# Performance work log

Hardware: AMD Instinct MI355X
Metric: run time of the kernel (lower is better)

Reference implementation:

```python
import jax, jax.numpy as jnp
import numpy as np

DT = 1.0
EPS = 1e-6


def setup_inputs() -> dict:
    key = jax.random.key(0)
    k1, k2, k3, k4 = jax.random.split(key, 4)
    batch, in_ch, out_ch, state_dim, T = 16, 256, 256, 256, 8192
    u = jax.random.normal(k1, (batch, in_ch, T), dtype=jnp.float32)
    raw_lambda = jax.random.normal(k2, (state_dim,), dtype=jnp.float32)
    B_c = jax.random.normal(k3, (in_ch, state_dim), dtype=jnp.float32) * (1.0 / in_ch ** 0.5)
    C = jax.random.normal(k4, (state_dim, out_ch), dtype=jnp.float32) * (1.0 / state_dim ** 0.5)
    return {"u": u, "raw_lambda": raw_lambda, "B_c": B_c, "C": C}


def reference(u, raw_lambda, B_c, C):
    # ZOH discretization of diagonal SSM (all-real here since raw_lambda is real)
    lam = -jax.nn.softplus(raw_lambda)                 # (N,)
    A_d = jnp.exp(lam * DT)                            # (N,)
    factor = jnp.where(jnp.abs(lam) > EPS, (A_d - 1.0) / lam, jnp.full_like(lam, DT))
    B_d = B_c * factor[None, :]                        # (in_ch, N)

    # Precompute driving inputs for every step in one big GEMM: (T, B, N)
    x = jnp.einsum('bct,cn->tbn', u, B_d)

    batch, state_dim = u.shape[0], raw_lambda.shape[0]

    def step(s, x_t):
        s = s * A_d[None, :] + x_t                     # diagonal recurrence
        return s, s

    s0 = jnp.zeros((batch, state_dim), dtype=u.dtype)
    _, states = jax.lax.scan(step, s0, x)              # states: (T, B, N)

    # Project all states at once: y (B, out_ch, T)
    y = jnp.einsum('tbn,no->bot', states, C)
    return y
```

## Files before the change

kernel.cpp:

```cpp
#include <hip/hip_runtime.h>
#include <math.h>

typedef __attribute__((ext_vector_type(4)))  float f32x4;
typedef __attribute__((ext_vector_type(8)))  short short8;
typedef __attribute__((ext_vector_type(16))) float f32x16;

#define B_  16
#define C_  256
#define N_  256
#define O_  256
#define T_  8192
#define L_  64
#define NC_ 128

#define GLL16(gptr, lptr) \
  __builtin_amdgcn_global_load_lds((const __attribute__((address_space(1))) void*)(gptr), \
                                   (__attribute__((address_space(3))) void*)(lptr), 16, 0, 0)

__device__ inline unsigned short f2bf(float x) {
    unsigned u = __float_as_uint(x);
    u += 0x7fff + ((u >> 16) & 1);
    return (unsigned short)(u >> 16);
}
__device__ inline float bf2f(unsigned short h) {
    return __uint_as_float(((unsigned)h) << 16);
}
__device__ inline unsigned cvtpk(float a, float b) {
    unsigned r;
    asm("v_cvt_pk_bf16_f32 %0, %1, %2" : "=v"(r) : "v"(a), "v"(b));
    return r;
}
__device__ inline f32x16 zero16() {
    f32x16 z;
    #pragma unroll
    for (int i = 0; i < 16; ++i) z[i] = 0.f;
    return z;
}

__global__ __launch_bounds__(256) void k_prep(
    const float* __restrict__ raw_lambda, const float* __restrict__ B_c,
    const float* __restrict__ Cmat,
    float* __restrict__ Ad, float* __restrict__ AL,
    unsigned short* __restrict__ BdKf, unsigned short* __restrict__ CKf)
{
    const int r = blockIdx.x;
    const int t = threadIdx.x;
    const int kk = r >> 5, ri = r & 31;
    const int s = ri >> 4, hi = (ri >> 3) & 1, j = ri & 7;
    const int nt = t >> 5, l = (hi << 5) | (t & 31);
    const int idx = (((kk * 8 + nt) * 2 + s) * 64 + l) * 8 + j;

    if (blockIdx.y == 0) {
        const float x  = raw_lambda[t];
        const float sp = (x > 20.f) ? x : log1pf(expf(x));
        const float lam = -sp;
        const float ad  = expf(lam);
        const float factor = (fabsf(lam) > 1e-6f) ? (ad - 1.f) / lam : 1.f;
        if (r == 0) {
            Ad[t] = ad;
            float al = ad;
            #pragma unroll
            for (int i = 0; i < 6; ++i) al *= al;
            AL[t] = al;
        }
        BdKf[idx] = f2bf(B_c[r * N_ + t] * factor);
    } else {
        CKf[idx] = f2bf(Cmat[r * O_ + t]);
    }
}

#define LDFRAG(MAT, kk, buf) { \
    _Pragma("unroll") \
    for (int q_ = 0; q_ < 2; ++q_) \
        _Pragma("unroll") \
        for (int s_ = 0; s_ < 2; ++s_) \
            fb[buf][q_ * 2 + s_] = *(const short8*)( \
                (MAT) + ((((kk) * 8 + 2 * w + q_) * 2 + s_) * 64 + l) * 8); }

__global__ __launch_bounds__(256, 3) void k_phaseA(
    const float* __restrict__ u, const unsigned short* __restrict__ BdKf,
    const float* __restrict__ Ad, float* __restrict__ p_last,
    unsigned short* __restrict__ X, int doX)
{
    __shared__ __align__(16) unsigned short ut[16896];

    const int k = blockIdx.x, b = blockIdx.y;
    const int tid = threadIdx.x;
    const int w = tid >> 6, l = tid & 63, lo = l & 31, hi = l >> 5;
    const float* ub = u + (size_t)b * C_ * T_ + k * L_;

    const float adq0 = Ad[(2 * w + 0) * 32 + lo];
    const float adq1 = Ad[(2 * w + 1) * 32 + lo];

    {
        f32x4 va[8], vb[8];
        #pragma unroll
        for (int q = 0; q < 8; ++q) {
            const int idx = q * 256 + tid;
            const int p = idx >> 4, t4 = idx & 15;
            const float* base = ub + (size_t)(2 * p) * T_ + t4 * 4;
            va[q] = __builtin_nontemporal_load((const f32x4*)(base));
            vb[q] = __builtin_nontemporal_load((const f32x4*)(base + T_));
        }
        unsigned* ud = (unsigned*)ut;
        #pragma unroll
        for (int q = 0; q < 8; ++q) {
            const int idx = q * 256 + tid;
            const int p = idx >> 4, t4 = idx & 15;
            const int nb = p >> 2, jd = p & 3;
            #pragma unroll
            for (int r = 0; r < 4; ++r) {
                const int tA = 4 * t4 + r;
                const int xsw = (tA >> 3) & 3;
                ud[tA * 132 + (((nb ^ xsw) << 2) | jd)] = cvtpk(va[q][r], vb[q][r]);
            }
        }
    }
    __syncthreads();

    f32x16 a00 = zero16(), a01 = zero16(), a10 = zero16(), a11 = zero16();
    {
        short8 fb[3][4];
        LDFRAG(BdKf, 0, 0)
        LDFRAG(BdKf, 1, 1)
        #pragma unroll
        for (int kk = 0; kk < 8; ++kk) {
            if (kk < 6) LDFRAG(BdKf, kk + 2, (kk + 2) % 3)
            #pragma unroll
            for (int s = 0; s < 2; ++s) {
                const int blk8 = kk * 4 + s * 2 + hi;
                const int tA2 = lo, tB2 = 32 + lo;
                const short8 fa0 = *(const short8*)(ut + tA2 * 264 + ((blk8 ^ ((tA2 >> 3) & 3)) << 3));
                const short8 fa1 = *(const short8*)(ut + tB2 * 264 + ((blk8 ^ ((tB2 >> 3) & 3)) << 3));
                const short8 fb0 = fb[kk % 3][0 * 2 + s];
                const short8 fb1 = fb[kk % 3][1 * 2 + s];
                a00 = __builtin_amdgcn_mfma_f32_32x32x16_bf16(fa0, fb0, a00, 0, 0, 0);
                a01 = __builtin_amdgcn_mfma_f32_32x32x16_bf16(fa0, fb1, a01, 0, 0, 0);
                a10 = __builtin_amdgcn_mfma_f32_32x32x16_bf16(fa1, fb0, a10, 0, 0, 0);
                a11 = __builtin_amdgcn_mfma_f32_32x32x16_bf16(fa1, fb1, a11, 0, 0, 0);
            }
        }
    }

    if (doX) {
        unsigned* Xd = (unsigned*)X + (size_t)(k * B_ + b) * 8192;
        #pragma unroll
        for (int f = 0; f < 4; ++f) {
            const f32x16 a = (f == 0) ? a00 : (f == 1) ? a01 : (f == 2) ? a10 : a11;
            unsigned dw[8];
            #pragma unroll
            for (int d = 0; d < 8; ++d)
                dw[d] = cvtpk(a[2 * d], a[2 * d + 1]);
            unsigned* base = Xd + w * 2048 + f * 512 + l * 4;
            *(int4*)(base)       = *(const int4*)&dw[0];
            *(int4*)(base + 256) = *(const int4*)&dw[4];
        }
    }

    {
        float p[2];
        #pragma unroll
        for (int q = 0; q < 2; ++q) {
            const float ad = q ? adq1 : adq0;
            const float ad2 = ad * ad, ad4 = ad2 * ad2, ad8 = ad4 * ad4;
            const float ad16 = ad8 * ad8, ad32 = ad16 * ad16;
            float full[2];
            #pragma unroll
            for (int tt = 0; tt < 2; ++tt) {
                const f32x16 a = (tt == 0) ? (q == 0 ? a00 : a01)
                                           : (q == 0 ? a10 : a11);
                float v2[4];
                #pragma unroll
                for (int g = 0; g < 4; ++g)
                    v2[g] = fmaf(fmaf(fmaf(a[4*g], ad, a[4*g+1]), ad, a[4*g+2]), ad, a[4*g+3]);
                const float H = fmaf(fmaf(fmaf(v2[0], ad8, v2[1]), ad8, v2[2]), ad8, v2[3]);
                float P = hi ? H : H * ad4;
                P += __shfl_xor(P, 32);
                full[tt] = P;
            }
            p[q] = fmaf(full[0], ad32, full[1]);
        }
        if (hi == 0) {
            float* dst = p_last + (size_t)(k * B_ + b) * N_;
            dst[(2 * w + 0) * 32 + lo] = p[0];
            dst[(2 * w + 1) * 32 + lo] = p[1];
        }
    }
}

__global__ __launch_bounds__(256) void k_phaseB(
    const float* __restrict__ p_last, const float* __restrict__ AL,
    float* __restrict__ carry)
{
    __shared__ float buf[32 * 256];
    const int b = blockIdx.x, n = threadIdx.x;
    const float al = AL[n];
    float cur = 0.f;
    for (int kc = 0; kc < 4; ++kc) {
        __syncthreads();
        #pragma unroll
        for (int q = 0; q < 32; ++q)
            buf[q * 256 + n] = p_last[((size_t)(kc * 32 + q) * B_ + b) * N_ + n];
        __syncthreads();
        #pragma unroll
        for (int q = 0; q < 32; ++q) {
            carry[((size_t)(kc * 32 + q) * B_ + b) * N_ + n] = cur;
            cur = fmaf(cur, al, buf[q * 256 + n]);
        }
    }
}

__global__ __launch_bounds__(256, 3) void k_phaseC(
    const unsigned short* __restrict__ X, const unsigned short* __restrict__ CKf,
    const float* __restrict__ Ad, const float* __restrict__ carry,
    float* __restrict__ y)
{
    __shared__ __align__(16) unsigned short xs[16896];

    const int k = blockIdx.x, b = blockIdx.y;
    const int tid = threadIdx.x;
    const int w = tid >> 6, l = tid & 63, lo = l & 31, hi = l >> 5;
    const int t0 = k * L_;

    {
        const char* src = (const char*)X + (size_t)(k * B_ + b) * 32768;
        #pragma unroll
        for (int q = 0; q < 8; ++q)
            GLL16(src + q * 4096 + w * 1024 + (l << 4),
                  (char*)xs + q * 4096 + w * 1024);
    }
    const float cv = carry[(size_t)(k * B_ + b) * N_ + tid];
    const float ad = Ad[tid];
    __syncthreads();

    unsigned arr[2][2][8];
    {
        const unsigned* xd = (const unsigned*)xs;
        const int w2 = tid >> 6, q2 = (tid >> 5) & 1, lo2 = tid & 31;
        #pragma unroll
        for (int tt = 0; tt < 2; ++tt)
            #pragma unroll
            for (int h2 = 0; h2 < 2; ++h2) {
                const unsigned* p = xd + w2 * 2048 + (tt * 2 + q2) * 512
                                       + (h2 * 32 + lo2) * 4;
                *(int4*)&arr[tt][h2][0] = *(const int4*)(p);
                *(int4*)&arr[tt][h2][4] = *(const int4*)(p + 256);
            }
    }
    __syncthreads();

    {
        const int nb = tid >> 3, nl = tid & 7;
        float s = cv;
        #pragma unroll
        for (int tt = 0; tt < 2; ++tt)
            #pragma unroll
            for (int g = 0; g < 4; ++g)
                #pragma unroll
                for (int h2 = 0; h2 < 2; ++h2) {
                    const unsigned d0 = arr[tt][h2][2 * g];
                    const unsigned d1 = arr[tt][h2][2 * g + 1];
                    const int tb = tt * 32 + 8 * g + 4 * h2;
                    const int swz = (((nb ^ ((tb >> 3) & 3)) << 3) | nl);
                    s = fmaf(s, ad, bf2f((unsigned short)(d0 & 0xffff)));
                    xs[(tb + 0) * 264 + swz] = f2bf(s);
                    s = fmaf(s, ad, bf2f((unsigned short)(d0 >> 16)));
                    xs[(tb + 1) * 264 + swz] = f2bf(s);
                    s = fmaf(s, ad, bf2f((unsigned short)(d1 & 0xffff)));
                    xs[(tb + 2) * 264 + swz] = f2bf(s);
                    s = fmaf(s, ad, bf2f((unsigned short)(d1 >> 16)));
                    xs[(tb + 3) * 264 + swz] = f2bf(s);
                }
    }
    __syncthreads();

    f32x16 c00 = zero16(), c01 = zero16(), c10 = zero16(), c11 = zero16();
    {
        short8 fb[3][4];
        LDFRAG(CKf, 0, 0)
        LDFRAG(CKf, 1, 1)
        #pragma unroll
        for (int kk = 0; kk < 8; ++kk) {
            if (kk < 6) LDFRAG(CKf, kk + 2, (kk + 2) % 3)
            #pragma unroll
            for (int s = 0; s < 2; ++s) {
                short8 fa[2];
                #pragma unroll
                for (int tt = 0; tt < 2; ++tt) {
                    const int t = tt * 32 + lo;
                    const int blk = (kk * 4 + s * 2 + hi) ^ ((t >> 3) & 3);
                    fa[tt] = *(const short8*)(xs + t * 264 + blk * 8);
                }
                const short8 fb0 = fb[kk % 3][0 * 2 + s];
                const short8 fb1 = fb[kk % 3][1 * 2 + s];
                c00 = __builtin_amdgcn_mfma_f32_32x32x16_bf16(fa[0], fb0, c00, 0, 0, 0);
                c01 = __builtin_amdgcn_mfma_f32_32x32x16_bf16(fa[0], fb1, c01, 0, 0, 0);
                c10 = __builtin_amdgcn_mfma_f32_32x32x16_bf16(fa[1], fb0, c10, 0, 0, 0);
                c11 = __builtin_amdgcn_mfma_f32_32x32x16_bf16(fa[1], fb1, c11, 0, 0, 0);
            }
        }
    }

    #pragma unroll
    for (int tt = 0; tt < 2; ++tt)
        #pragma unroll
        for (int q = 0; q < 2; ++q) {
            const f32x16 a = (tt == 0) ? (q == 0 ? c00 : c01) : (q == 0 ? c10 : c11);
            const int o = (2 * w + q) * 32 + lo;
            float* yo = y + ((size_t)b * O_ + o) * T_ + t0 + tt * 32 + hi * 4;
            #pragma unroll
            for (int g = 0; g < 4; ++g) {
                float4 vv;
                vv.x = a[g * 4 + 0]; vv.y = a[g * 4 + 1];
                vv.z = a[g * 4 + 2]; vv.w = a[g * 4 + 3];
                *(float4*)(yo + g * 8) = vv;
            }
        }
}

__device__ __forceinline__ void gemm1_rc(
    const float* __restrict__ u, const unsigned short* __restrict__ BdKf,
    int b, int k, unsigned short* xs, unsigned short* ut, unsigned short* bb)
{
    const int tid = threadIdx.x;
    const int w = tid >> 6, l = tid & 63, lo = l & 31, hi = l >> 5;
    const int t0 = k * L_;
    f32x16 a00 = zero16(), a01 = zero16(), a10 = zero16(), a11 = zero16();
    for (int kk = 0; kk < 8; ++kk) {
        #pragma unroll
        for (int q = 0; q < 2; ++q) {
            const int i = q * 256 + tid, cl = i >> 4, t4 = i & 15;
            const float4 v = *(const float4*)(
                u + ((size_t)b * C_ + kk * 32 + cl) * T_ + t0 + t4 * 4);
            ut[(t4 * 4 + 0) * 40 + cl] = f2bf(v.x);
            ut[(t4 * 4 + 1) * 40 + cl] = f2bf(v.y);
            ut[(t4 * 4 + 2) * 40 + cl] = f2bf(v.z);
            ut[(t4 * 4 + 3) * 40 + cl] = f2bf(v.w);
        }
        {
            const unsigned short* src = BdKf + kk * 8192;
            #pragma unroll
            for (int q = 0; q < 4; ++q) {
                const int i16 = q * 256 + tid;
                *(int4*)(bb + i16 * 8) = *(const int4*)(src + i16 * 8);
            }
        }
        __syncthreads();
        #pragma unroll
        for (int s = 0; s < 2; ++s) {
            const short8 fa0 = *(const short8*)(ut + (0 * 32 + lo) * 40 + s * 16 + hi * 8);
            const short8 fa1 = *(const short8*)(ut + (1 * 32 + lo) * 40 + s * 16 + hi * 8);
            const short8 fb0 = *(const short8*)(bb + (((2 * w + 0) * 2 + s) * 64 + l) * 8);
            const short8 fb1 = *(const short8*)(bb + (((2 * w + 1) * 2 + s) * 64 + l) * 8);
            a00 = __builtin_amdgcn_mfma_f32_32x32x16_bf16(fa0, fb0, a00, 0, 0, 0);
            a01 = __builtin_amdgcn_mfma_f32_32x32x16_bf16(fa0, fb1, a01, 0, 0, 0);
            a10 = __builtin_amdgcn_mfma_f32_32x32x16_bf16(fa1, fb0, a10, 0, 0, 0);
            a11 = __builtin_amdgcn_mfma_f32_32x32x16_bf16(fa1, fb1, a11, 0, 0, 0);
        }
        __syncthreads();
    }
    #pragma unroll
    for (int tt = 0; tt < 2; ++tt)
        #pragma unroll
        for (int q = 0; q < 2; ++q) {
            const f32x16 a = (tt == 0) ? (q == 0 ? a00 : a01) : (q == 0 ? a10 : a11);
            const int n = (2 * w + q) * 32 + lo;
            #pragma unroll
            for (int g = 0; g < 4; ++g)
                #pragma unroll
                for (int p = 0; p < 2; ++p)
                    *(unsigned*)(xs + n * 66 + tt * 32 + hi * 4 + g * 8 + p * 2)
                        = f2bf(a[g * 4 + 2 * p]) | ((unsigned)f2bf(a[g * 4 + 2 * p + 1]) << 16);
        }
    __syncthreads();
}

__global__ __launch_bounds__(256) void k_phaseC_rc(
    const float* __restrict__ u, const unsigned short* __restrict__ BdKf,
    const unsigned short* __restrict__ CKf, const float* __restrict__ Ad,
    const float* __restrict__ carry, float* __restrict__ y)
{
    __shared__ __align__(16) unsigned short xs[16896];
    __shared__ __align__(16) unsigned short ut[2560];
    __shared__ __align__(16) unsigned short bb[8192];

    const int k = blockIdx.x, b = blockIdx.y;
    const int tid = threadIdx.x;
    const int w = tid >> 6, l = tid & 63, lo = l & 31, hi = l >> 5;
    const int t0 = k * L_;

    gemm1_rc(u, BdKf, b, k, xs, ut, bb);

    {
        const float a = Ad[tid];
        float s = carry[((size_t)k * B_ + b) * N_ + tid];
        float st[64];
        #pragma unroll
        for (int m = 0; m < 32; ++m) {
            const unsigned dw = *(const unsigned*)(xs + tid * 66 + 2 * m);
            s = fmaf(s, a, bf2f((unsigned short)(dw & 0xffff)));  st[2 * m] = s;
            s = fmaf(s, a, bf2f((unsigned short)(dw >> 16)));     st[2 * m + 1] = s;
        }
        __syncthreads();
        #pragma unroll
        for (int t = 0; t < 64; ++t) xs[t * 264 + tid] = f2bf(st[t]);
    }
    __syncthreads();

    f32x16 c00 = zero16(), c01 = zero16(), c10 = zero16(), c11 = zero16();
    for (int kk = 0; kk < 8; ++kk) {
        __syncthreads();
        {
            const unsigned short* src = CKf + kk * 8192;
            #pragma unroll
            for (int q = 0; q < 4; ++q) {
                const int i16 = q * 256 + tid;
                *(int4*)(bb + i16 * 8) = *(const int4*)(src + i16 * 8);
            }
        }
        __syncthreads();
        #pragma unroll
        for (int s = 0; s < 2; ++s) {
            const short8 fa0 = *(const short8*)(xs + (0 * 32 + lo) * 264 + kk * 32 + s * 16 + hi * 8);
            const short8 fa1 = *(const short8*)(xs + (1 * 32 + lo) * 264 + kk * 32 + s * 16 + hi * 8);
            const short8 fb0 = *(const short8*)(bb + (((2 * w + 0) * 2 + s) * 64 + l) * 8);
            const short8 fb1 = *(const short8*)(bb + (((2 * w + 1) * 2 + s) * 64 + l) * 8);
            c00 = __builtin_amdgcn_mfma_f32_32x32x16_bf16(fa0, fb0, c00, 0, 0, 0);
            c01 = __builtin_amdgcn_mfma_f32_32x32x16_bf16(fa0, fb1, c01, 0, 0, 0);
            c10 = __builtin_amdgcn_mfma_f32_32x32x16_bf16(fa1, fb0, c10, 0, 0, 0);
            c11 = __builtin_amdgcn_mfma_f32_32x32x16_bf16(fa1, fb1, c11, 0, 0, 0);
        }
    }

    #pragma unroll
    for (int tt = 0; tt < 2; ++tt)
        #pragma unroll
        for (int q = 0; q < 2; ++q) {
            const f32x16 a = (tt == 0) ? (q == 0 ? c00 : c01) : (q == 0 ? c10 : c11);
            const int o = (2 * w + q) * 32 + lo;
            float* yo = y + ((size_t)b * O_ + o) * T_ + t0 + tt * 32 + hi * 4;
            #pragma unroll
            for (int g = 0; g < 4; ++g) {
                float4 vv;
                vv.x = a[g * 4 + 0]; vv.y = a[g * 4 + 1];
                vv.z = a[g * 4 + 2]; vv.w = a[g * 4 + 3];
                *(float4*)(yo + g * 8) = vv;
            }
        }
}

extern "C" void kernel_launch(void* const* d_in, const int* in_sizes, int n_in,
                              void* d_out, int out_size, void* d_ws, size_t ws_size,
                              hipStream_t stream)
{
    const float* u  = (const float*)d_in[0];
    const float* rl = (const float*)d_in[1];
    const float* Bc = (const float*)d_in[2];
    const float* Cm = (const float*)d_in[3];
    float* y  = (float*)d_out;
    char*  ws = (char*)d_ws;

    float* Ad     = (float*)(ws + 0);
    float* AL     = (float*)(ws + 1024);
    float* p_last = (float*)(ws + 2048);
    float* carry  = (float*)(ws + 2048 + 2097152);
    unsigned short* BdKf = (unsigned short*)(ws + 2048 + 2 * 2097152);
    unsigned short* CKf  = (unsigned short*)(ws + 2048 + 2 * 2097152 + 131072);
    unsigned short* X    = (unsigned short*)(ws + 2048 + 2 * 2097152 + 2 * 131072);
    const size_t need = 2048 + 2ull * 2097152 + 2ull * 131072
                      + (size_t)NC_ * B_ * 32768;
    const int doX = (ws_size >= need) ? 1 : 0;

    k_prep  <<<dim3(256, 2),  dim3(256), 0, stream>>>(rl, Bc, Cm, Ad, AL, BdKf, CKf);
    k_phaseA<<<dim3(NC_, B_), dim3(256), 0, stream>>>(u, BdKf, Ad, p_last, X, doX);
    k_phaseB<<<dim3(B_),      dim3(256), 0, stream>>>(p_last, AL, carry);
    if (doX)
        k_phaseC<<<dim3(NC_, B_), dim3(256), 0, stream>>>(X, CKf, Ad, carry, y);
    else
        k_phaseC_rc<<<dim3(NC_, B_), dim3(256), 0, stream>>>(u, BdKf, CKf, Ad, carry, y);
}
```

Baseline: 102.6 us.

## Warp-specialize phase A with double-buffered LDS over four chunks per block

Phase A now uses 512-thread blocks, where half the waves load and pack u into LDS while the other half run the MFMA GEMM and the X and p_last epilogues. Each block processes four consecutive chunks with a double-buffered LDS tile. The aim is to overlap the global loads of u with tensor-core compute and epilogue stores. The trade-offs are a grid four times smaller, more LDS per block, and a sync per chunk, which may reduce overall memory parallelism.

```diff
diff --git a/kernel.cpp b/kernel.cpp
--- a/kernel.cpp
+++ b/kernel.cpp
@@ -12,6 +12,7 @@
 #define T_  8192
 #define L_  64
 #define NC_ 128
+#define CH_ 4
 
 #define GLL16(gptr, lptr) \
   __builtin_amdgcn_global_load_lds((const __attribute__((address_space(1))) void*)(gptr), \
@@ -77,35 +78,33 @@
             fb[buf][q_ * 2 + s_] = *(const short8*)( \
                 (MAT) + ((((kk) * 8 + 2 * w + q_) * 2 + s_) * 64 + l) * 8); }
 
-__global__ __launch_bounds__(256, 3) void k_phaseA(
+__global__ __launch_bounds__(512) void k_phaseA(
     const float* __restrict__ u, const unsigned short* __restrict__ BdKf,
     const float* __restrict__ Ad, float* __restrict__ p_last,
     unsigned short* __restrict__ X, int doX)
 {
-    __shared__ __align__(16) unsigned short ut[16896];
-
-    const int k = blockIdx.x, b = blockIdx.y;
+    __shared__ __align__(16) unsigned short ut[2][16896];
+
+    const int k0 = blockIdx.x * CH_, b = blockIdx.y;
     const int tid = threadIdx.x;
-    const int w = tid >> 6, l = tid & 63, lo = l & 31, hi = l >> 5;
-    const float* ub = u + (size_t)b * C_ * T_ + k * L_;
-
-    const float adq0 = Ad[(2 * w + 0) * 32 + lo];
-    const float adq1 = Ad[(2 * w + 1) * 32 + lo];
-
-    {
+    const bool loader = tid < 256;
+    const float* ub = u + (size_t)b * C_ * T_ + k0 * L_;
+
+    const int lt = tid;
+    auto load_pack = [&](int chunk, unsigned short* dst) {
         f32x4 va[8], vb[8];
         #pragma unroll
         for (int q = 0; q < 8; ++q) {
-            const int idx = q * 256 + tid;
+            const int idx = q * 256 + lt;
             const int p = idx >> 4, t4 = idx & 15;
-            const float* base = ub + (size_t)(2 * p) * T_ + t4 * 4;
+            const float* base = ub + (size_t)(2 * p) * T_ + chunk * L_ + t4 * 4;
             va[q] = __builtin_nontemporal_load((const f32x4*)(base));
             vb[q] = __builtin_nontemporal_load((const f32x4*)(base + T_));
         }
-        unsigned* ud = (unsigned*)ut;
+        unsigned* ud = (unsigned*)dst;
         #pragma unroll
         for (int q = 0; q < 8; ++q) {
-            const int idx = q * 256 + tid;
+            const int idx = q * 256 + lt;
             const int p = idx >> 4, t4 = idx & 15;
             const int nb = p >> 2, jd = p & 3;
             #pragma unroll
@@ -115,11 +114,18 @@
                 ud[tA * 132 + (((nb ^ xsw) << 2) | jd)] = cvtpk(va[q][r], vb[q][r]);
             }
         }
-    }
-    __syncthreads();
-
-    f32x16 a00 = zero16(), a01 = zero16(), a10 = zero16(), a11 = zero16();
-    {
+    };
+
+    const int ct = tid - 256;
+    const int w = (ct >> 6) & 3, l = ct & 63, lo = l & 31, hi = l >> 5;
+    float adq0 = 0.f, adq1 = 0.f;
+    if (!loader) {
+        adq0 = Ad[(2 * w + 0) * 32 + lo];
+        adq1 = Ad[(2 * w + 1) * 32 + lo];
+    }
+
+    auto gemm = [&](const unsigned short* src,
+                    f32x16& a00, f32x16& a01, f32x16& a10, f32x16& a11) {
         short8 fb[3][4];
         LDFRAG(BdKf, 0, 0)
         LDFRAG(BdKf, 1, 1)
@@ -130,8 +136,8 @@
             for (int s = 0; s < 2; ++s) {
                 const int blk8 = kk * 4 + s * 2 + hi;
                 const int tA2 = lo, tB2 = 32 + lo;
-                const short8 fa0 = *(const short8*)(ut + tA2 * 264 + ((blk8 ^ ((tA2 >> 3) & 3)) << 3));
-                const short8 fa1 = *(const short8*)(ut + tB2 * 264 + ((blk8 ^ ((tB2 >> 3) & 3)) << 3));
+                const short8 fa0 = *(const short8*)(src + tA2 * 264 + ((blk8 ^ ((tA2 >> 3) & 3)) << 3));
+                const short8 fa1 = *(const short8*)(src + tB2 * 264 + ((blk8 ^ ((tB2 >> 3) & 3)) << 3));
                 const short8 fb0 = fb[kk % 3][0 * 2 + s];
                 const short8 fb1 = fb[kk % 3][1 * 2 + s];
                 a00 = __builtin_amdgcn_mfma_f32_32x32x16_bf16(fa0, fb0, a00, 0, 0, 0);
@@ -140,13 +146,14 @@
                 a11 = __builtin_amdgcn_mfma_f32_32x32x16_bf16(fa1, fb1, a11, 0, 0, 0);
             }
         }
-    }
-
-    if (doX) {
+    };
+
+    auto xstore = [&](const f32x16& a00, const f32x16& a01,
+                      const f32x16& a10, const f32x16& a11, int k) {
         unsigned* Xd = (unsigned*)X + (size_t)(k * B_ + b) * 8192;
         #pragma unroll
         for (int f = 0; f < 4; ++f) {
-            const f32x16 a = (f == 0) ? a00 : (f == 1) ? a01 : (f == 2) ? a10 : a11;
+            const f32x16& a = (f == 0) ? a00 : (f == 1) ? a01 : (f == 2) ? a10 : a11;
             unsigned dw[8];
             #pragma unroll
             for (int d = 0; d < 8; ++d)
@@ -155,9 +162,10 @@
             *(int4*)(base)       = *(const int4*)&dw[0];
             *(int4*)(base + 256) = *(const int4*)&dw[4];
         }
-    }
-
-    {
+    };
+
+    auto plast = [&](const f32x16& a00, const f32x16& a01,
+                     const f32x16& a10, const f32x16& a11, int k) {
         float p[2];
         #pragma unroll
         for (int q = 0; q < 2; ++q) {
@@ -167,8 +175,8 @@
             float full[2];
             #pragma unroll
             for (int tt = 0; tt < 2; ++tt) {
-                const f32x16 a = (tt == 0) ? (q == 0 ? a00 : a01)
-                                           : (q == 0 ? a10 : a11);
+                const f32x16& a = (tt == 0) ? (q == 0 ? a00 : a01)
+                                            : (q == 0 ? a10 : a11);
                 float v2[4];
                 #pragma unroll
                 for (int g = 0; g < 4; ++g)
@@ -185,6 +193,22 @@
             dst[(2 * w + 0) * 32 + lo] = p[0];
             dst[(2 * w + 1) * 32 + lo] = p[1];
         }
+    };
+
+    if (loader) load_pack(0, ut[0]);
+    __syncthreads();
+
+    #pragma unroll
+    for (int i = 0; i < CH_; ++i) {
+        if (loader) {
+            if (i + 1 < CH_) load_pack(i + 1, ut[(i + 1) & 1]);
+        } else {
+            f32x16 a00 = zero16(), a01 = zero16(), a10 = zero16(), a11 = zero16();
+            gemm(ut[i & 1], a00, a01, a10, a11);
+            if (doX) xstore(a00, a01, a10, a11, k0 + i);
+            plast(a00, a01, a10, a11, k0 + i);
+        }
+        __syncthreads();
     }
 }
 
@@ -472,10 +496,10 @@
     const int doX = (ws_size >= need) ? 1 : 0;
 
     k_prep  <<<dim3(256, 2),  dim3(256), 0, stream>>>(rl, Bc, Cm, Ad, AL, BdKf, CKf);
-    k_phaseA<<<dim3(NC_, B_), dim3(256), 0, stream>>>(u, BdKf, Ad, p_last, X, doX);
-    k_phaseB<<<dim3(B_),      dim3(256), 0, stream>>>(p_last, AL, carry);
+    k_phaseA<<<dim3(NC_ / CH_, B_), dim3(512), 0, stream>>>(u, BdKf, Ad, p_last, X, doX);
+    k_phaseB<<<dim3(B_),            dim3(256), 0, stream>>>(p_last, AL, carry);
     if (doX)
-        k_phaseC<<<dim3(NC_, B_), dim3(256), 0, stream>>>(X, CKf, Ad, carry, y);
+        k_phaseC<<<dim3(NC_, B_),   dim3(256), 0, stream>>>(X, CKf, Ad, carry, y);
     else
         k_phaseC_rc<<<dim3(NC_, B_), dim3(256), 0, stream>>>(u, BdKf, CKf, Ad, carry, y);
 }
```

Measured after the change: 105.9 us. 3.2% more time.
